# Optimization experiments

Measured on AMD Instinct MI355X. Metric: run time of the kernel, lower is better.

The kernel has to match this reference:

```python
import jax, jax.numpy as jnp
import numpy as np

D, L, C, H, W = 4, 16, 64, 128, 128


def setup_inputs() -> dict:
    key = jax.random.key(0)
    ks = jax.random.split(key, 20)
    rn = lambda k, shape, s=0.02: jax.random.normal(k, shape, dtype=jnp.float32) * s
    return {
        "x": jax.random.normal(ks[0], (L, C, H, W), dtype=jnp.float32),
        "ln1_g": jnp.ones((D, C, H, W), jnp.float32),
        "ln1_b": jnp.zeros((D, C, H, W), jnp.float32),
        "Wq": rn(ks[1], (D, C, C)), "bq": jnp.zeros((D, C), jnp.float32),
        "Wk": rn(ks[2], (D, C, C)), "bk": jnp.zeros((D, C), jnp.float32),
        "Wv": rn(ks[3], (D, C, C)), "bv": jnp.zeros((D, C), jnp.float32),
        "Wa": rn(ks[4], (D, 1, 2 * C, 5, 5)), "ba": jnp.zeros((D, 1), jnp.float32),
        "ln2_g": jnp.ones((D, C, H, W), jnp.float32),
        "ln2_b": jnp.zeros((D, C, H, W), jnp.float32),
        "W1": rn(ks[5], (D, 2 * C, C)), "b1": jnp.zeros((D, 2 * C), jnp.float32),
        "W2": rn(ks[6], (D, C, 2 * C)), "b2": jnp.zeros((D, C), jnp.float32),
    }


def _layernorm(x, g, b):
    # torch nn.LayerNorm([C,H,W]): normalize over last 3 dims per frame, eps=1e-5
    mu = jnp.mean(x, axis=(1, 2, 3), keepdims=True)
    var = jnp.var(x, axis=(1, 2, 3), keepdims=True)
    return (x - mu) * jax.lax.rsqrt(var + 1e-5) * g[None] + b[None]


def _conv5(x, w):
    # x: [L, Cin, H, W], w: [1, Cin, 5, 5] -> [L, 1, H, W], SAME padding (pad=2)
    return jax.lax.conv_general_dilated(
        x, w, window_strides=(1, 1), padding="SAME",
        dimension_numbers=("NCHW", "OIHW", "NCHW"))


def _conv1x1(x, w, b):
    # 1x1 conv == per-pixel linear over channels
    return jnp.einsum("lchw,oc->lohw", x, w) + b[None, :, None, None]


def reference(x, ln1_g, ln1_b, Wq, bq, Wk, bk, Wv, bv, Wa, ba,
              ln2_g, ln2_b, W1, b1, W2, b2):
    depth = ln1_g.shape[0]
    c = Wa.shape[2] // 2
    for d in range(depth):
        # --- pre-norm conv attention (nheads=1) + residual ---
        h = _layernorm(x, ln1_g[d], ln1_b[d])
        Q = _conv1x1(h, Wq[d], bq[d])
        K = _conv1x1(h, Wk[d], bk[d])
        V = _conv1x1(h, Wv[d], bv[d])
        # conv_atten(cat([Q_i, K_j])) is linear in channels: split the 5x5
        # kernel into Q-part and K-part, so H_ij = A_i + B_j + bias.
        A = _conv5(Q, Wa[d, :, :c])[:, 0]   # [L, H, W]
        B = _conv5(K, Wa[d, :, c:])[:, 0]   # [L, H, W]
        S = A[:, None] + B[None, :] + ba[d][0]      # [L, L, H, W]
        P = jax.nn.softmax(S, axis=1)               # softmax over source frames j
        attn = jnp.einsum("ijhw,jchw->ichw", P, V)  # weighted sum of V_j
        x = x + attn
        # --- pre-norm conv FFN + residual ---
        h = _layernorm(x, ln2_g[d], ln2_b[d])
        f = _conv1x1(h, W1[d], b1[d])
        f = jax.nn.leaky_relu(f, 0.01)  # torch LeakyReLU default slope
        f = _conv1x1(f, W2[d], b2[d])
        x = x + f
    return x
```

## Files before the change

### kernel.cpp

```cpp
#include <hip/hip_runtime.h>


#define HW 16384
#define CHW 1048576
#define NB 64

typedef unsigned short u16;
typedef __attribute__((ext_vector_type(8))) short bf16x8;
typedef __attribute__((ext_vector_type(8))) unsigned short u16x8;
typedef __attribute__((ext_vector_type(4))) float f32x4;

static __device__ __forceinline__ u16 f2bf(float f) {
  union { float f; unsigned int u; } v; v.f = f;
  unsigned int r = v.u + 0x7fffu + ((v.u >> 16) & 1u);
  return (u16)(r >> 16);
}
static __device__ __forceinline__ float bf2f(u16 h) {
  union { unsigned int u; float f; } v; v.u = ((unsigned int)h) << 16;
  return v.f;
}
static __device__ __forceinline__ void ln_from_acc_wave(
    const float* acc, int l, int lane, float& mu, float& r) {
  const float invN = 1.f / 1048576.f;
  float2 v = *(const float2*)(acc + lane * 32 + 2 * l);
  float s = v.x, q = v.y;
#pragma unroll
  for (int off = 32; off > 0; off >>= 1) {
    s += __shfl_xor(s, off);
    q += __shfl_xor(q, off);
  }
  mu = s * invN;
  r = rsqrtf(q * invN - mu * mu + 1e-5f);
}

__global__ __launch_bounds__(256) void prep_kernel(
    const float* __restrict__ Wa, const float* __restrict__ Wk,
    const float* __restrict__ Wv, const float* __restrict__ W1,
    const float* __restrict__ W2, u16* __restrict__ w1pk,
    u16* __restrict__ w2pk, u16* __restrict__ wvpk, u16* __restrict__ wepk) {
  int d = blockIdx.x;
  int t = blockIdx.y * 256 + threadIdx.x;
  const int STR = 256 * 16;
  const float* WaK = Wa + ((size_t)d * 128 + 64) * 25;
  const float* Wkd = Wk + d * 4096;
  for (int idx = t; idx < 2048; idx += STR) {
    int frag = idx >> 9, lane = (idx >> 3) & 63, j = idx & 7;
    int mt = frag >> 1, kt = frag & 1;
    int tap = mt * 16 + (lane & 15);
    int ci = kt * 32 + (lane >> 4) * 8 + j;
    float s = 0.f;
    if (tap < 25)
      for (int co = 0; co < 64; ++co)
        s = fmaf(WaK[co * 25 + tap], Wkd[co * 64 + ci], s);
    wepk[d * 2048 + idx] = f2bf(s);
  }
  const float* Wvd = Wv + d * 4096;
  for (int idx = t; idx < 4096; idx += STR) {
    int frag = idx >> 9, lane = (idx >> 3) & 63, j = idx & 7;
    int mt = frag >> 1, kt = frag & 1;
    int co = mt * 16 + (lane & 15);
    int ci = kt * 32 + (lane >> 4) * 8 + j;
    wvpk[d * 4096 + idx] = f2bf(Wvd[co * 64 + ci]);
  }
  const float* W1d = W1 + d * 8192;
  for (int idx = t; idx < 8192; idx += STR) {
    int frag = idx >> 9, lane = (idx >> 3) & 63, j = idx & 7;
    int mt = frag >> 1, kt = frag & 1;
    int o = mt * 16 + (lane & 15);
    int ci = kt * 32 + (lane >> 4) * 8 + j;
    w1pk[d * 8192 + idx] = f2bf(W1d[o * 64 + ci]);
  }
  const float* W2d = W2 + d * 8192;
  for (int idx = t; idx < 8192; idx += STR) {
    int frag = idx >> 9, lane = (idx >> 3) & 63, j = idx & 7;
    int mt2 = frag >> 2, kt2 = frag & 3;
    int c = mt2 * 16 + (lane & 15);
    int o = kt2 * 32 + (lane >> 4) * 8 + j;
    w2pk[d * 8192 + idx] = f2bf(W2d[c * 128 + o]);
  }
}

__global__ __launch_bounds__(256) void stats_kernel(
    const float* __restrict__ xin, float* __restrict__ acc) {
  int tid = threadIdx.x;
  size_t base = (size_t)blockIdx.x * 4096;
  const float4* in4 = (const float4*)(xin + base);
  float s = 0.f, q = 0.f;
#pragma unroll
  for (int k = 0; k < 4; ++k) {
    float4 v = in4[k * 256 + tid];
    s += v.x + v.y + v.z + v.w;
    q = fmaf(v.x, v.x, q); q = fmaf(v.y, v.y, q);
    q = fmaf(v.z, v.z, q); q = fmaf(v.w, v.w, q);
  }
#pragma unroll
  for (int off = 32; off > 0; off >>= 1) {
    s += __shfl_down(s, off); q += __shfl_down(q, off);
  }
  __shared__ float ls[4], lq[4];
  int wave = tid >> 6;
  if ((tid & 63) == 0) { ls[wave] = s; lq[wave] = q; }
  __syncthreads();
  if (tid == 0) {
    int frame = blockIdx.x >> 8;
    int bkt = blockIdx.x & (NB - 1);
    atomicAdd(&acc[bkt * 32 + frame * 2], ls[0] + ls[1] + ls[2] + ls[3]);
    atomicAdd(&acc[bkt * 32 + frame * 2 + 1], lq[0] + lq[1] + lq[2] + lq[3]);
  }
}

__global__ __launch_bounds__(256) void vb_kernel(
    const float* __restrict__ x, const float* __restrict__ g,
    const float* __restrict__ bln, const u16* __restrict__ wvp_g,
    const float* __restrict__ bv, const u16* __restrict__ wep_g,
    const float* __restrict__ accA, float* __restrict__ accBz,
    u16* __restrict__ Vb, u16* __restrict__ T) {
  __shared__ __align__(16) char lds[18432];
  u16* hb = (u16*)lds;
  int tid = threadIdx.x;
  int l = blockIdx.y;
  int p0 = blockIdx.x << 7;
  if (blockIdx.x == 0 && blockIdx.y == 0)
    for (int i = tid; i < NB * 32; i += 256) accBz[i] = 0.f;
  int lane = tid & 63;
  float mu, r;
  ln_from_acc_wave(accA, l, lane, mu, r);

#pragma unroll
  for (int it = 0; it < 2; ++it) {
    int pq = tid & 31, cg = (tid >> 5) + it * 8;
    int px = pq * 4, c0 = cg * 4;
    float vv[4][4];
#pragma unroll
    for (int i = 0; i < 4; ++i) {
      int c = c0 + i;
      size_t gi = (((size_t)l * 64 + c) << 14) + p0 + px;
      int li = (c << 14) + p0 + px;
      float4 xv = *(const float4*)(x + gi);
      float4 gv = *(const float4*)(g + li);
      float4 bb = *(const float4*)(bln + li);
      vv[i][0] = (xv.x - mu) * r * gv.x + bb.x;
      vv[i][1] = (xv.y - mu) * r * gv.y + bb.y;
      vv[i][2] = (xv.z - mu) * r * gv.z + bb.z;
      vv[i][3] = (xv.w - mu) * r * gv.w + bb.w;
    }
#pragma unroll
    for (int k = 0; k < 4; ++k) {
      int row = px + k;
      int col = ((((c0 >> 3) + (row >> 2)) & 7) << 3) | (c0 & 7);
      ushort4 hv;
      hv.x = f2bf(vv[0][k]); hv.y = f2bf(vv[1][k]);
      hv.z = f2bf(vv[2][k]); hv.w = f2bf(vv[3][k]);
      *(ushort4*)(hb + row * 72 + col) = hv;
    }
  }
  __syncthreads();

  int wv = tid >> 6;
  int ln15 = lane & 15, quad = lane >> 4;

  bf16x8 ah[2][2];
#pragma unroll
  for (int mt = 0; mt < 2; ++mt) {
    int px = (wv * 2 + mt) * 16 + ln15;
#pragma unroll
    for (int kt = 0; kt < 2; ++kt) {
      int slot = ((kt * 4 + quad) + (px >> 2)) & 7;
      ah[mt][kt] = *(const bf16x8*)(hb + px * 72 + (slot << 3));
    }
  }
  const bf16x8* wvg = (const bf16x8*)wvp_g;
  const bf16x8* weg = (const bf16x8*)wep_g;

  f32x4 accV[2][4], accT[2][2];
#pragma unroll
  for (int mt = 0; mt < 2; ++mt) {
#pragma unroll
    for (int nt = 0; nt < 4; ++nt) accV[mt][nt] = (f32x4){0.f, 0.f, 0.f, 0.f};
#pragma unroll
    for (int nt = 0; nt < 2; ++nt) accT[mt][nt] = (f32x4){0.f, 0.f, 0.f, 0.f};
  }
#pragma unroll
  for (int nt = 0; nt < 4; ++nt) {
    bf16x8 b0 = wvg[(nt * 2 + 0) * 64 + lane];
    bf16x8 b1w = wvg[(nt * 2 + 1) * 64 + lane];
#pragma unroll
    for (int mt = 0; mt < 2; ++mt) {
      accV[mt][nt] = __builtin_amdgcn_mfma_f32_16x16x32_bf16(
          ah[mt][0], b0, accV[mt][nt], 0, 0, 0);
      accV[mt][nt] = __builtin_amdgcn_mfma_f32_16x16x32_bf16(
          ah[mt][1], b1w, accV[mt][nt], 0, 0, 0);
    }
  }
#pragma unroll
  for (int nt = 0; nt < 2; ++nt) {
    bf16x8 b0 = weg[(nt * 2 + 0) * 64 + lane];
    bf16x8 b1w = weg[(nt * 2 + 1) * 64 + lane];
#pragma unroll
    for (int mt = 0; mt < 2; ++mt) {
      accT[mt][nt] = __builtin_amdgcn_mfma_f32_16x16x32_bf16(
          ah[mt][0], b0, accT[mt][nt], 0, 0, 0);
      accT[mt][nt] = __builtin_amdgcn_mfma_f32_16x16x32_bf16(
          ah[mt][1], b1w, accT[mt][nt], 0, 0, 0);
    }
  }

#pragma unroll
  for (int mt = 0; mt < 2; ++mt) {
    int pxb = p0 + (wv * 2 + mt) * 16 + quad * 4;
#pragma unroll
    for (int nt = 0; nt < 4; ++nt) {
      int c = nt * 16 + ln15;
      float bvc = bv[c];
      ushort4 o;
      o.x = f2bf(accV[mt][nt][0] + bvc);
      o.y = f2bf(accV[mt][nt][1] + bvc);
      o.z = f2bf(accV[mt][nt][2] + bvc);
      o.w = f2bf(accV[mt][nt][3] + bvc);
      *(ushort4*)(Vb + (((size_t)l * 64 + c) << 14) + pxb) = o;
    }
#pragma unroll
    for (int nt = 0; nt < 2; ++nt) {
      int tap = nt * 16 + ln15;
      if (tap < 25) {
        ushort4 o;
        o.x = f2bf(accT[mt][nt][0]); o.y = f2bf(accT[mt][nt][1]);
        o.z = f2bf(accT[mt][nt][2]); o.w = f2bf(accT[mt][nt][3]);
        *(ushort4*)(T + (((size_t)l * 25 + tap) << 14) + pxb) = o;
      }
    }
  }
}

__global__ __launch_bounds__(256) void bconv_kernel(
    const u16* __restrict__ T, float* __restrict__ B) {
  int gid = blockIdx.x * 256 + threadIdx.x;
  int l = gid >> 14, p = gid & 16383;
  int y = p >> 7, xx = p & 127;
  float s = 0.f;
#pragma unroll
  for (int dy = 0; dy < 5; ++dy) {
    int yy = y + dy - 2;
    if (yy < 0 || yy > 127) continue;
#pragma unroll
    for (int dx = 0; dx < 5; ++dx) {
      int xc = xx + dx - 2;
      if (xc < 0 || xc > 127) continue;
      s += bf2f(T[(((size_t)l * 25 + dy * 5 + dx) << 14) + (yy << 7) + xc]);
    }
  }
  B[gid] = s;
}

__global__ __launch_bounds__(256) void attnc_update_kernel(
    const float* __restrict__ x, const u16* __restrict__ Vb,
    const float* __restrict__ B, float* __restrict__ ap,
    float* __restrict__ accB, float* __restrict__ accAz) {
  int tid = threadIdx.x;
  if (blockIdx.x == 0)
    for (int i = tid; i < NB * 32; i += 256) accAz[i] = 0.f;
  int gid = blockIdx.x * 256 + tid;
  int c = gid >> 11;
  int p8 = (gid & 2047) << 3;
  float m[8];
#pragma unroll
  for (int k = 0; k < 8; ++k) m[k] = -1e30f;
#pragma unroll
  for (int j = 0; j < 16; ++j) {
    float4 b0 = *(const float4*)(B + (j << 14) + p8);
    float4 b1 = *(const float4*)(B + (j << 14) + p8 + 4);
    m[0] = fmaxf(m[0], b0.x); m[1] = fmaxf(m[1], b0.y);
    m[2] = fmaxf(m[2], b0.z); m[3] = fmaxf(m[3], b0.w);
    m[4] = fmaxf(m[4], b1.x); m[5] = fmaxf(m[5], b1.y);
    m[6] = fmaxf(m[6], b1.z); m[7] = fmaxf(m[7], b1.w);
  }
  float sum[8], a[8];
#pragma unroll
  for (int k = 0; k < 8; ++k) { sum[k] = 0.f; a[k] = 0.f; }
#pragma unroll
  for (int j = 0; j < 16; ++j) {
    float4 b0 = *(const float4*)(B + (j << 14) + p8);
    float4 b1 = *(const float4*)(B + (j << 14) + p8 + 4);
    float e[8];
    e[0] = __expf(b0.x - m[0]); e[1] = __expf(b0.y - m[1]);
    e[2] = __expf(b0.z - m[2]); e[3] = __expf(b0.w - m[3]);
    e[4] = __expf(b1.x - m[4]); e[5] = __expf(b1.y - m[5]);
    e[6] = __expf(b1.z - m[6]); e[7] = __expf(b1.w - m[7]);
    u16x8 v = *(const u16x8*)(Vb + (((size_t)j * 64 + c) << 14) + p8);
#pragma unroll
    for (int k = 0; k < 8; ++k) {
      sum[k] += e[k];
      a[k] = fmaf(e[k], bf2f(v[k]), a[k]);
    }
  }
#pragma unroll
  for (int k = 0; k < 8; ++k) a[k] /= sum[k];
  float4 a0 = {a[0], a[1], a[2], a[3]};
  float4 a1 = {a[4], a[5], a[6], a[7]};
  *(float4*)(ap + ((size_t)c << 14) + p8) = a0;
  *(float4*)(ap + ((size_t)c << 14) + p8 + 4) = a1;
  float sf[16], qf[16];
#pragma unroll
  for (int f = 0; f < 16; ++f) {
    size_t gi = ((size_t)f << 20) + ((size_t)c << 14) + p8;
    float4 v0 = *(const float4*)(x + gi);
    float4 v1 = *(const float4*)(x + gi + 4);
    v0.x += a0.x; v0.y += a0.y; v0.z += a0.z; v0.w += a0.w;
    v1.x += a1.x; v1.y += a1.y; v1.z += a1.z; v1.w += a1.w;
    sf[f] = v0.x + v0.y + v0.z + v0.w + v1.x + v1.y + v1.z + v1.w;
    float q = 0.f;
    q = fmaf(v0.x, v0.x, q); q = fmaf(v0.y, v0.y, q);
    q = fmaf(v0.z, v0.z, q); q = fmaf(v0.w, v0.w, q);
    q = fmaf(v1.x, v1.x, q); q = fmaf(v1.y, v1.y, q);
    q = fmaf(v1.z, v1.z, q); q = fmaf(v1.w, v1.w, q);
    qf[f] = q;
  }
#pragma unroll
  for (int off = 32; off > 0; off >>= 1) {
#pragma unroll
    for (int f = 0; f < 16; ++f) {
      sf[f] += __shfl_down(sf[f], off);
      qf[f] += __shfl_down(qf[f], off);
    }
  }
  __shared__ float lsq[4][32];
  int wv = tid >> 6;
  if ((tid & 63) == 0) {
#pragma unroll
    for (int f = 0; f < 16; ++f) {
      lsq[wv][2 * f] = sf[f];
      lsq[wv][2 * f + 1] = qf[f];
    }
  }
  __syncthreads();
  if (tid < 32) {
    int bkt = blockIdx.x & (NB - 1);
    atomicAdd(&accB[bkt * 32 + tid],
              lsq[0][tid] + lsq[1][tid] + lsq[2][tid] + lsq[3][tid]);
  }
}

__global__ __launch_bounds__(256) void ffn_kernel(
    const float* __restrict__ xr, float* __restrict__ xw,
    const float* __restrict__ ap, const float* __restrict__ g,
    const float* __restrict__ bln, const u16* __restrict__ w1p_g,
    const float* __restrict__ b1, const u16* __restrict__ w2p_g,
    const float* __restrict__ b2, const float* __restrict__ accB,
    float* __restrict__ accA) {
  __shared__ __align__(16) char lds[66560];
  float* xaf = (float*)lds;
  u16* hb = (u16*)(lds + 33792);
  u16* f1 = (u16*)(lds + 33792);

  int tid = threadIdx.x;
  int P0 = blockIdx.x << 7;
  int l = P0 >> 14;
  int p0 = P0 & 16383;
  int lane = tid & 63;
  float mu, r;
  ln_from_acc_wave(accB, l, lane, mu, r);

#pragma unroll
  for (int it = 0; it < 2; ++it) {
    int pq = tid & 31, cg = (tid >> 5) + it * 8;
    int px = pq * 4, c0 = cg * 4;
    float vv[4][4];
#pragma unroll
    for (int i = 0; i < 4; ++i) {
      int c = c0 + i;
      size_t gi = (((size_t)l * 64 + c) << 14) + p0 + px;
      int li = (c << 14) + p0 + px;
      float4 xv = *(const float4*)(xr + gi);
      float4 av = *(const float4*)(ap + li);
      float4 gv = *(const float4*)(g + li);
      float4 bb = *(const float4*)(bln + li);
      float4 s4;
      s4.x = xv.x + av.x; s4.y = xv.y + av.y;
      s4.z = xv.z + av.z; s4.w = xv.w + av.w;
      *(float4*)(xaf + c * 132 + px) = s4;
      vv[i][0] = (s4.x - mu) * r * gv.x + bb.x;
      vv[i][1] = (s4.y - mu) * r * gv.y + bb.y;
      vv[i][2] = (s4.z - mu) * r * gv.z + bb.z;
      vv[i][3] = (s4.w - mu) * r * gv.w + bb.w;
    }
#pragma unroll
    for (int k = 0; k < 4; ++k) {
      int row = px + k;
      int col = ((((c0 >> 3) + (row >> 2)) & 7) << 3) | (c0 & 7);
      ushort4 hv;
      hv.x = f2bf(vv[0][k]); hv.y = f2bf(vv[1][k]);
      hv.z = f2bf(vv[2][k]); hv.w = f2bf(vv[3][k]);
      *(ushort4*)(hb + row * 72 + col) = hv;
    }
  }
  __syncthreads();

  int wv = tid >> 6;
  int ln15 = lane & 15, quad = lane >> 4;

  bf16x8 bh[2][2];
#pragma unroll
  for (int nt = 0; nt < 2; ++nt) {
    int px = (wv * 2 + nt) * 16 + ln15;
#pragma unroll
    for (int kt = 0; kt < 2; ++kt) {
      int slot = ((kt * 4 + quad) + (px >> 2)) & 7;
      bh[nt][kt] = *(const bf16x8*)(hb + px * 72 + (slot << 3));
    }
  }
  __syncthreads();

  const bf16x8* w1g = (const bf16x8*)w1p_g;
  const bf16x8* w2g = (const bf16x8*)w2p_g;

#pragma unroll
  for (int mt = 0; mt < 8; ++mt) {
    bf16x8 a1a = w1g[(mt * 2 + 0) * 64 + lane];
    bf16x8 a1b = w1g[(mt * 2 + 1) * 64 + lane];
    f32x4 acc[2];
    acc[0] = (f32x4){0.f, 0.f, 0.f, 0.f};
    acc[1] = (f32x4){0.f, 0.f, 0.f, 0.f};
#pragma unroll
    for (int nt = 0; nt < 2; ++nt) {
      acc[nt] = __builtin_amdgcn_mfma_f32_16x16x32_bf16(a1a, bh[nt][0],
                                                        acc[nt], 0, 0, 0);
      acc[nt] = __builtin_amdgcn_mfma_f32_16x16x32_bf16(a1b, bh[nt][1],
                                                        acc[nt], 0, 0, 0);
    }
    int o0 = mt * 16 + quad * 4;
    float4 b1v = *(const float4*)(b1 + o0);
#pragma unroll
    for (int nt = 0; nt < 2; ++nt) {
      int px = (wv * 2 + nt) * 16 + ln15;
      int swz = (px & 7) * 8;
      float fv[4];
#pragma unroll
      for (int rj = 0; rj < 4; ++rj) {
        float f = acc[nt][rj] + ((const float*)&b1v)[rj];
        fv[rj] = fmaxf(f, 0.01f * f);
      }
      int col = ((o0 & ~7) ^ swz) + (o0 & 7);
      ushort4 ov;
      ov.x = f2bf(fv[0]); ov.y = f2bf(fv[1]);
      ov.z = f2bf(fv[2]); ov.w = f2bf(fv[3]);
      *(ushort4*)(f1 + px * 128 + col) = ov;
    }
  }
  __syncthreads();

  bf16x8 a2[2][4];
#pragma unroll
  for (int mt = 0; mt < 2; ++mt) {
    int px = (wv * 2 + mt) * 16 + ln15;
    int swz = (px & 7) * 8;
#pragma unroll
    for (int kt = 0; kt < 4; ++kt)
      a2[mt][kt] =
          *(const bf16x8*)(f1 + px * 128 + ((kt * 32 + quad * 8) ^ swz));
  }
  f32x4 acc2[2][4];
#pragma unroll
  for (int mt = 0; mt < 2; ++mt)
#pragma unroll
    for (int nt = 0; nt < 4; ++nt) acc2[mt][nt] = (f32x4){0.f, 0.f, 0.f, 0.f};
#pragma unroll
  for (int nt = 0; nt < 4; ++nt) {
    bf16x8 bw[4];
#pragma unroll
    for (int kt = 0; kt < 4; ++kt) bw[kt] = w2g[(nt * 4 + kt) * 64 + lane];
#pragma unroll
    for (int mt = 0; mt < 2; ++mt)
#pragma unroll
      for (int kt = 0; kt < 4; ++kt)
        acc2[mt][nt] = __builtin_amdgcn_mfma_f32_16x16x32_bf16(
            a2[mt][kt], bw[kt], acc2[mt][nt], 0, 0, 0);
  }

  float s = 0.f, q = 0.f;
#pragma unroll
  for (int mt = 0; mt < 2; ++mt) {
    int pxl = (wv * 2 + mt) * 16 + quad * 4;
#pragma unroll
    for (int nt = 0; nt < 4; ++nt) {
      int c = nt * 16 + ln15;
      float b2c = b2[c];
      const float* xac = xaf + c * 132 + pxl;
      float4 v;
      v.x = xac[0] + acc2[mt][nt][0] + b2c;
      v.y = xac[1] + acc2[mt][nt][1] + b2c;
      v.z = xac[2] + acc2[mt][nt][2] + b2c;
      v.w = xac[3] + acc2[mt][nt][3] + b2c;
      *(float4*)(xw + (((size_t)l * 64 + c) << 14) + p0 + pxl) = v;
      s += v.x + v.y + v.z + v.w;
      q = fmaf(v.x, v.x, q); q = fmaf(v.y, v.y, q);
      q = fmaf(v.z, v.z, q); q = fmaf(v.w, v.w, q);
    }
  }
#pragma unroll
  for (int off = 32; off > 0; off >>= 1) {
    s += __shfl_down(s, off); q += __shfl_down(q, off);
  }
  if (lane == 0) {
    int bkt = blockIdx.x & (NB - 1);
    atomicAdd(&accA[bkt * 32 + l * 2], s);
    atomicAdd(&accA[bkt * 32 + l * 2 + 1], q);
  }
}

extern "C" void kernel_launch(void* const* d_in, const int* in_sizes, int n_in,
                              void* d_out, int out_size, void* d_ws,
                              size_t ws_size, hipStream_t stream) {
  const float* x_in = (const float*)d_in[0];
  const float* ln1_g = (const float*)d_in[1];
  const float* ln1_b = (const float*)d_in[2];
  const float* Wk = (const float*)d_in[5];
  const float* Wv = (const float*)d_in[7];
  const float* bv = (const float*)d_in[8];
  const float* Wa = (const float*)d_in[9];
  const float* ln2_g = (const float*)d_in[11];
  const float* ln2_b = (const float*)d_in[12];
  const float* W1 = (const float*)d_in[13];
  const float* b1 = (const float*)d_in[14];
  const float* W2 = (const float*)d_in[15];
  const float* b2 = (const float*)d_in[16];

  float* xbuf = (float*)d_out;
  char* wsb = (char*)d_ws;
  u16* Vb = (u16*)wsb;
  u16* T = (u16*)(wsb + 33554432);
  float* aplane = (float*)(wsb + 46661632);
  float* Bbuf = (float*)(wsb + 50855936);
  u16* w1pk = (u16*)(wsb + 51904512);
  u16* w2pk = (u16*)(wsb + 51970048);
  u16* wvpk = (u16*)(wsb + 52035584);
  u16* wepk = (u16*)(wsb + 52068352);
  float* accA = (float*)(wsb + 52084736);
  float* accB = (float*)(wsb + 52092928);

  hipMemsetAsync(accA, 0, 16384, stream);
  prep_kernel<<<dim3(4, 16), 256, 0, stream>>>(Wa, Wk, Wv, W1, W2, w1pk, w2pk,
                                               wvpk, wepk);
  stats_kernel<<<4096, 256, 0, stream>>>(x_in, accA);

  const float* xr = x_in;
  for (int d = 0; d < 4; ++d) {
    vb_kernel<<<dim3(128, 16), 256, 0, stream>>>(
        xr, ln1_g + (size_t)d * CHW, ln1_b + (size_t)d * CHW, wvpk + d * 4096,
        bv + d * 64, wepk + d * 2048, accA, accB, Vb, T);
    bconv_kernel<<<1024, 256, 0, stream>>>(T, Bbuf);
    attnc_update_kernel<<<512, 256, 0, stream>>>(xr, Vb, Bbuf, aplane, accB,
                                                 accA);
    ffn_kernel<<<2048, 256, 0, stream>>>(
        xr, xbuf, aplane, ln2_g + (size_t)d * CHW, ln2_b + (size_t)d * CHW,
        w1pk + d * 8192, b1 + d * 128, w2pk + d * 8192, b2 + d * 64, accB,
        accA);
    xr = xbuf;
  }
}
```

Measured before the change: 598.8 us.

## Apply softmax weights before V projection and store LN params in bf16

```diff
diff --git a/kernel.cpp b/kernel.cpp
--- a/kernel.cpp
+++ b/kernel.cpp
@@ -80,6 +80,26 @@
   }
 }
 
+__global__ __launch_bounds__(256) void lngb_kernel(
+    const float* __restrict__ g1, const float* __restrict__ b1,
+    const float* __restrict__ g2, const float* __restrict__ b2,
+    u16* __restrict__ o1, u16* __restrict__ o2, u16* __restrict__ o3,
+    u16* __restrict__ o4) {
+  int idx = blockIdx.x * 256 + threadIdx.x;
+  const float* src;
+  u16* dst;
+  switch (blockIdx.y) {
+    case 0: src = g1; dst = o1; break;
+    case 1: src = b1; dst = o2; break;
+    case 2: src = g2; dst = o3; break;
+    default: src = b2; dst = o4; break;
+  }
+  float4 v = *(const float4*)(src + (size_t)idx * 4);
+  ushort4 o;
+  o.x = f2bf(v.x); o.y = f2bf(v.y); o.z = f2bf(v.z); o.w = f2bf(v.w);
+  *(ushort4*)(dst + (size_t)idx * 4) = o;
+}
+
 __global__ __launch_bounds__(256) void stats_kernel(
     const float* __restrict__ xin, float* __restrict__ acc) {
   int tid = threadIdx.x;
@@ -109,12 +129,11 @@
   }
 }
 
-__global__ __launch_bounds__(256) void vb_kernel(
-    const float* __restrict__ x, const float* __restrict__ g,
-    const float* __restrict__ bln, const u16* __restrict__ wvp_g,
-    const float* __restrict__ bv, const u16* __restrict__ wep_g,
+__global__ __launch_bounds__(256) void tb_kernel(
+    const float* __restrict__ x, const u16* __restrict__ g,
+    const u16* __restrict__ bln, const u16* __restrict__ wep_g,
     const float* __restrict__ accA, float* __restrict__ accBz,
-    u16* __restrict__ Vb, u16* __restrict__ T) {
+    float* __restrict__ mulr, u16* __restrict__ T) {
   __shared__ __align__(16) char lds[18432];
   u16* hb = (u16*)lds;
   int tid = threadIdx.x;
@@ -125,6 +144,10 @@
   int lane = tid & 63;
   float mu, r;
   ln_from_acc_wave(accA, l, lane, mu, r);
+  if (blockIdx.x == 0 && tid == 0) {
+    mulr[2 * l] = mu;
+    mulr[2 * l + 1] = r;
+  }
 
 #pragma unroll
   for (int it = 0; it < 2; ++it) {
@@ -137,12 +160,12 @@
       size_t gi = (((size_t)l * 64 + c) << 14) + p0 + px;
       int li = (c << 14) + p0 + px;
       float4 xv = *(const float4*)(x + gi);
-      float4 gv = *(const float4*)(g + li);
-      float4 bb = *(const float4*)(bln + li);
-      vv[i][0] = (xv.x - mu) * r * gv.x + bb.x;
-      vv[i][1] = (xv.y - mu) * r * gv.y + bb.y;
-      vv[i][2] = (xv.z - mu) * r * gv.z + bb.z;
-      vv[i][3] = (xv.w - mu) * r * gv.w + bb.w;
+      ushort4 gv = *(const ushort4*)(g + li);
+      ushort4 bb = *(const ushort4*)(bln + li);
+      vv[i][0] = (xv.x - mu) * r * bf2f(gv.x) + bf2f(bb.x);
+      vv[i][1] = (xv.y - mu) * r * bf2f(gv.y) + bf2f(bb.y);
+      vv[i][2] = (xv.z - mu) * r * bf2f(gv.z) + bf2f(bb.z);
+      vv[i][3] = (xv.w - mu) * r * bf2f(gv.w) + bf2f(bb.w);
     }
 #pragma unroll
     for (int k = 0; k < 4; ++k) {
@@ -169,29 +192,13 @@
       ah[mt][kt] = *(const bf16x8*)(hb + px * 72 + (slot << 3));
     }
   }
-  const bf16x8* wvg = (const bf16x8*)wvp_g;
   const bf16x8* weg = (const bf16x8*)wep_g;
 
-  f32x4 accV[2][4], accT[2][2];
-#pragma unroll
-  for (int mt = 0; mt < 2; ++mt) {
-#pragma unroll
-    for (int nt = 0; nt < 4; ++nt) accV[mt][nt] = (f32x4){0.f, 0.f, 0.f, 0.f};
+  f32x4 accT[2][2];
+#pragma unroll
+  for (int mt = 0; mt < 2; ++mt)
 #pragma unroll
     for (int nt = 0; nt < 2; ++nt) accT[mt][nt] = (f32x4){0.f, 0.f, 0.f, 0.f};
-  }
-#pragma unroll
-  for (int nt = 0; nt < 4; ++nt) {
-    bf16x8 b0 = wvg[(nt * 2 + 0) * 64 + lane];
-    bf16x8 b1w = wvg[(nt * 2 + 1) * 64 + lane];
-#pragma unroll
-    for (int mt = 0; mt < 2; ++mt) {
-      accV[mt][nt] = __builtin_amdgcn_mfma_f32_16x16x32_bf16(
-          ah[mt][0], b0, accV[mt][nt], 0, 0, 0);
-      accV[mt][nt] = __builtin_amdgcn_mfma_f32_16x16x32_bf16(
-          ah[mt][1], b1w, accV[mt][nt], 0, 0, 0);
-    }
-  }
 #pragma unroll
   for (int nt = 0; nt < 2; ++nt) {
     bf16x8 b0 = weg[(nt * 2 + 0) * 64 + lane];
@@ -208,17 +215,6 @@
 #pragma unroll
   for (int mt = 0; mt < 2; ++mt) {
     int pxb = p0 + (wv * 2 + mt) * 16 + quad * 4;
-#pragma unroll
-    for (int nt = 0; nt < 4; ++nt) {
-      int c = nt * 16 + ln15;
-      float bvc = bv[c];
-      ushort4 o;
-      o.x = f2bf(accV[mt][nt][0] + bvc);
-      o.y = f2bf(accV[mt][nt][1] + bvc);
-      o.z = f2bf(accV[mt][nt][2] + bvc);
-      o.w = f2bf(accV[mt][nt][3] + bvc);
-      *(ushort4*)(Vb + (((size_t)l * 64 + c) << 14) + pxb) = o;
-    }
 #pragma unroll
     for (int nt = 0; nt < 2; ++nt) {
       int tap = nt * 16 + ln15;
@@ -252,68 +248,139 @@
   B[gid] = s;
 }
 
-__global__ __launch_bounds__(256) void attnc_update_kernel(
-    const float* __restrict__ x, const u16* __restrict__ Vb,
-    const float* __restrict__ B, float* __restrict__ ap,
+__global__ __launch_bounds__(256) void attnc_kernel(
+    const float* __restrict__ x, const float* __restrict__ B,
+    const u16* __restrict__ g1, const u16* __restrict__ b1g,
+    const u16* __restrict__ wvp_g, const float* __restrict__ bv,
+    const float* __restrict__ mulr, u16* __restrict__ abf,
     float* __restrict__ accB, float* __restrict__ accAz) {
+  __shared__ float Prl[16][64];
+  __shared__ float scal[64];
+  __shared__ __align__(16) u16 hb[64 * 72];
+  __shared__ float lsq[4][32];
   int tid = threadIdx.x;
+  int p0 = blockIdx.x << 6;
   if (blockIdx.x == 0)
     for (int i = tid; i < NB * 32; i += 256) accAz[i] = 0.f;
-  int gid = blockIdx.x * 256 + tid;
-  int c = gid >> 11;
-  int p8 = (gid & 2047) << 3;
-  float m[8];
-#pragma unroll
-  for (int k = 0; k < 8; ++k) m[k] = -1e30f;
+
+  if (tid < 64) {
+    float bj[16], m = -1e30f;
+#pragma unroll
+    for (int j = 0; j < 16; ++j) {
+      bj[j] = B[(j << 14) + p0 + tid];
+      m = fmaxf(m, bj[j]);
+    }
+    float sum = 0.f;
+#pragma unroll
+    for (int j = 0; j < 16; ++j) {
+      bj[j] = __expf(bj[j] - m);
+      sum += bj[j];
+    }
+    float inv = 1.f / sum;
+    float sc = 0.f;
+#pragma unroll
+    for (int j = 0; j < 16; ++j) {
+      float mu_j = mulr[2 * j], r_j = mulr[2 * j + 1];
+      float prl = bj[j] * inv * r_j;
+      Prl[j][tid] = prl;
+      sc = fmaf(prl, mu_j, sc);
+    }
+    scal[tid] = sc;
+  }
+  __syncthreads();
+
+  int csub = tid >> 4, pxq = tid & 15;
+  f32x4 xbar[4];
+#pragma unroll
+  for (int cc = 0; cc < 4; ++cc) xbar[cc] = (f32x4){0.f, 0.f, 0.f, 0.f};
 #pragma unroll
   for (int j = 0; j < 16; ++j) {
-    float4 b0 = *(const float4*)(B + (j << 14) + p8);
-    float4 b1 = *(const float4*)(B + (j << 14) + p8 + 4);
-    m[0] = fmaxf(m[0], b0.x); m[1] = fmaxf(m[1], b0.y);
-    m[2] = fmaxf(m[2], b0.z); m[3] = fmaxf(m[3], b0.w);
-    m[4] = fmaxf(m[4], b1.x); m[5] = fmaxf(m[5], b1.y);
-    m[6] = fmaxf(m[6], b1.z); m[7] = fmaxf(m[7], b1.w);
-  }
-  float sum[8], a[8];
-#pragma unroll
-  for (int k = 0; k < 8; ++k) { sum[k] = 0.f; a[k] = 0.f; }
-#pragma unroll
-  for (int j = 0; j < 16; ++j) {
-    float4 b0 = *(const float4*)(B + (j << 14) + p8);
-    float4 b1 = *(const float4*)(B + (j << 14) + p8 + 4);
-    float e[8];
-    e[0] = __expf(b0.x - m[0]); e[1] = __expf(b0.y - m[1]);
-    e[2] = __expf(b0.z - m[2]); e[3] = __expf(b0.w - m[3]);
-    e[4] = __expf(b1.x - m[4]); e[5] = __expf(b1.y - m[5]);
-    e[6] = __expf(b1.z - m[6]); e[7] = __expf(b1.w - m[7]);
-    u16x8 v = *(const u16x8*)(Vb + (((size_t)j * 64 + c) << 14) + p8);
-#pragma unroll
-    for (int k = 0; k < 8; ++k) {
-      sum[k] += e[k];
-      a[k] = fmaf(e[k], bf2f(v[k]), a[k]);
-    }
-  }
-#pragma unroll
-  for (int k = 0; k < 8; ++k) a[k] /= sum[k];
-  float4 a0 = {a[0], a[1], a[2], a[3]};
-  float4 a1 = {a[4], a[5], a[6], a[7]};
-  *(float4*)(ap + ((size_t)c << 14) + p8) = a0;
-  *(float4*)(ap + ((size_t)c << 14) + p8 + 4) = a1;
+    f32x4 P4 = *(const f32x4*)&Prl[j][pxq * 4];
+#pragma unroll
+    for (int cc = 0; cc < 4; ++cc) {
+      int c = cc * 16 + csub;
+      float4 xv =
+          *(const float4*)(x + (((size_t)j * 64 + c) << 14) + p0 + pxq * 4);
+      xbar[cc][0] = fmaf(P4[0], xv.x, xbar[cc][0]);
+      xbar[cc][1] = fmaf(P4[1], xv.y, xbar[cc][1]);
+      xbar[cc][2] = fmaf(P4[2], xv.z, xbar[cc][2]);
+      xbar[cc][3] = fmaf(P4[3], xv.w, xbar[cc][3]);
+    }
+  }
+  {
+    f32x4 sc4 = *(const f32x4*)&scal[pxq * 4];
+#pragma unroll
+    for (int cc = 0; cc < 4; ++cc) {
+      int c = cc * 16 + csub;
+      ushort4 g4 = *(const ushort4*)(g1 + ((size_t)c << 14) + p0 + pxq * 4);
+      ushort4 b4 = *(const ushort4*)(b1g + ((size_t)c << 14) + p0 + pxq * 4);
+      float hv[4];
+      hv[0] = bf2f(g4.x) * (xbar[cc][0] - sc4[0]) + bf2f(b4.x);
+      hv[1] = bf2f(g4.y) * (xbar[cc][1] - sc4[1]) + bf2f(b4.y);
+      hv[2] = bf2f(g4.z) * (xbar[cc][2] - sc4[2]) + bf2f(b4.z);
+      hv[3] = bf2f(g4.w) * (xbar[cc][3] - sc4[3]) + bf2f(b4.w);
+#pragma unroll
+      for (int k = 0; k < 4; ++k) {
+        int row = pxq * 4 + k;
+        int col = ((((c >> 3) + (row >> 2)) & 7) << 3) | (c & 7);
+        hb[row * 72 + col] = f2bf(hv[k]);
+      }
+    }
+  }
+  __syncthreads();
+
+  int wv = tid >> 6, lane = tid & 63;
+  int ln15 = lane & 15, quad = lane >> 4;
+  int px = wv * 16 + ln15;
+  bf16x8 ah[2];
+#pragma unroll
+  for (int kt = 0; kt < 2; ++kt) {
+    int slot = ((kt * 4 + quad) + (px >> 2)) & 7;
+    ah[kt] = *(const bf16x8*)(hb + px * 72 + (slot << 3));
+  }
+  const bf16x8* wvg = (const bf16x8*)wvp_g;
+  f32x4 accV[4];
+#pragma unroll
+  for (int nt = 0; nt < 4; ++nt) accV[nt] = (f32x4){0.f, 0.f, 0.f, 0.f};
+#pragma unroll
+  for (int nt = 0; nt < 4; ++nt) {
+    bf16x8 b0 = wvg[(nt * 2 + 0) * 64 + lane];
+    bf16x8 b1w = wvg[(nt * 2 + 1) * 64 + lane];
+    accV[nt] = __builtin_amdgcn_mfma_f32_16x16x32_bf16(ah[0], b0, accV[nt],
+                                                       0, 0, 0);
+    accV[nt] = __builtin_amdgcn_mfma_f32_16x16x32_bf16(ah[1], b1w, accV[nt],
+                                                       0, 0, 0);
+  }
+  int pxb = p0 + wv * 16 + quad * 4;
+  float av[4][4];
+#pragma unroll
+  for (int nt = 0; nt < 4; ++nt) {
+    int c = nt * 16 + ln15;
+    float bvc = bv[c];
+    ushort4 o;
+    av[nt][0] = accV[nt][0] + bvc; o.x = f2bf(av[nt][0]);
+    av[nt][1] = accV[nt][1] + bvc; o.y = f2bf(av[nt][1]);
+    av[nt][2] = accV[nt][2] + bvc; o.z = f2bf(av[nt][2]);
+    av[nt][3] = accV[nt][3] + bvc; o.w = f2bf(av[nt][3]);
+    *(ushort4*)(abf + ((size_t)c << 14) + pxb) = o;
+  }
+
   float sf[16], qf[16];
 #pragma unroll
   for (int f = 0; f < 16; ++f) {
-    size_t gi = ((size_t)f << 20) + ((size_t)c << 14) + p8;
-    float4 v0 = *(const float4*)(x + gi);
-    float4 v1 = *(const float4*)(x + gi + 4);
-    v0.x += a0.x; v0.y += a0.y; v0.z += a0.z; v0.w += a0.w;
-    v1.x += a1.x; v1.y += a1.y; v1.z += a1.z; v1.w += a1.w;
-    sf[f] = v0.x + v0.y + v0.z + v0.w + v1.x + v1.y + v1.z + v1.w;
-    float q = 0.f;
-    q = fmaf(v0.x, v0.x, q); q = fmaf(v0.y, v0.y, q);
-    q = fmaf(v0.z, v0.z, q); q = fmaf(v0.w, v0.w, q);
-    q = fmaf(v1.x, v1.x, q); q = fmaf(v1.y, v1.y, q);
-    q = fmaf(v1.z, v1.z, q); q = fmaf(v1.w, v1.w, q);
-    qf[f] = q;
+    float s = 0.f, q = 0.f;
+#pragma unroll
+    for (int nt = 0; nt < 4; ++nt) {
+      int c = nt * 16 + ln15;
+      float4 xv =
+          *(const float4*)(x + ((size_t)f << 20) + ((size_t)c << 14) + pxb);
+      float v0 = xv.x + av[nt][0], v1 = xv.y + av[nt][1];
+      float v2 = xv.z + av[nt][2], v3 = xv.w + av[nt][3];
+      s += v0 + v1 + v2 + v3;
+      q = fmaf(v0, v0, q); q = fmaf(v1, v1, q);
+      q = fmaf(v2, v2, q); q = fmaf(v3, v3, q);
+    }
+    sf[f] = s; qf[f] = q;
   }
 #pragma unroll
   for (int off = 32; off > 0; off >>= 1) {
@@ -323,9 +390,7 @@
       qf[f] += __shfl_down(qf[f], off);
     }
   }
-  __shared__ float lsq[4][32];
-  int wv = tid >> 6;
-  if ((tid & 63) == 0) {
+  if (lane == 0) {
 #pragma unroll
     for (int f = 0; f < 16; ++f) {
       lsq[wv][2 * f] = sf[f];
@@ -342,8 +407,8 @@
 
 __global__ __launch_bounds__(256) void ffn_kernel(
     const float* __restrict__ xr, float* __restrict__ xw,
-    const float* __restrict__ ap, const float* __restrict__ g,
-    const float* __restrict__ bln, const u16* __restrict__ w1p_g,
+    const u16* __restrict__ ap, const u16* __restrict__ g,
+    const u16* __restrict__ bln, const u16* __restrict__ w1p_g,
     const float* __restrict__ b1, const u16* __restrict__ w2p_g,
     const float* __restrict__ b2, const float* __restrict__ accB,
     float* __restrict__ accA) {
@@ -371,17 +436,17 @@
       size_t gi = (((size_t)l * 64 + c) << 14) + p0 + px;
       int li = (c << 14) + p0 + px;
       float4 xv = *(const float4*)(xr + gi);
-      float4 av = *(const float4*)(ap + li);
-      float4 gv = *(const float4*)(g + li);
-      float4 bb = *(const float4*)(bln + li);
+      ushort4 av4 = *(const ushort4*)(ap + li);
+      ushort4 gv = *(const ushort4*)(g + li);
+      ushort4 bb = *(const ushort4*)(bln + li);
       float4 s4;
-      s4.x = xv.x + av.x; s4.y = xv.y + av.y;
-      s4.z = xv.z + av.z; s4.w = xv.w + av.w;
+      s4.x = xv.x + bf2f(av4.x); s4.y = xv.y + bf2f(av4.y);
+      s4.z = xv.z + bf2f(av4.z); s4.w = xv.w + bf2f(av4.w);
       *(float4*)(xaf + c * 132 + px) = s4;
-      vv[i][0] = (s4.x - mu) * r * gv.x + bb.x;
-      vv[i][1] = (s4.y - mu) * r * gv.y + bb.y;
-      vv[i][2] = (s4.z - mu) * r * gv.z + bb.z;
-      vv[i][3] = (s4.w - mu) * r * gv.w + bb.w;
+      vv[i][0] = (s4.x - mu) * r * bf2f(gv.x) + bf2f(bb.x);
+      vv[i][1] = (s4.y - mu) * r * bf2f(gv.y) + bf2f(bb.y);
+      vv[i][2] = (s4.z - mu) * r * bf2f(gv.z) + bf2f(bb.z);
+      vv[i][3] = (s4.w - mu) * r * bf2f(gv.w) + bf2f(bb.w);
     }
 #pragma unroll
     for (int k = 0; k < 4; ++k) {
@@ -526,32 +591,39 @@
 
   float* xbuf = (float*)d_out;
   char* wsb = (char*)d_ws;
-  u16* Vb = (u16*)wsb;
-  u16* T = (u16*)(wsb + 33554432);
-  float* aplane = (float*)(wsb + 46661632);
-  float* Bbuf = (float*)(wsb + 50855936);
-  u16* w1pk = (u16*)(wsb + 51904512);
-  u16* w2pk = (u16*)(wsb + 51970048);
-  u16* wvpk = (u16*)(wsb + 52035584);
-  u16* wepk = (u16*)(wsb + 52068352);
-  float* accA = (float*)(wsb + 52084736);
-  float* accB = (float*)(wsb + 52092928);
+  u16* T = (u16*)wsb;
+  u16* abf = (u16*)(wsb + 13107200);
+  float* Bbuf = (float*)(wsb + 15204352);
+  u16* g1b = (u16*)(wsb + 16252928);
+  u16* b1bb = (u16*)(wsb + 24641536);
+  u16* g2b = (u16*)(wsb + 33030144);
+  u16* b2bb = (u16*)(wsb + 41418752);
+  u16* w1pk = (u16*)(wsb + 49807360);
+  u16* w2pk = (u16*)(wsb + 49872896);
+  u16* wvpk = (u16*)(wsb + 49938432);
+  u16* wepk = (u16*)(wsb + 49971200);
+  float* mulr = (float*)(wsb + 49987584);
+  float* accA = (float*)(wsb + 49987712);
+  float* accB = (float*)(wsb + 49995904);
 
   hipMemsetAsync(accA, 0, 16384, stream);
   prep_kernel<<<dim3(4, 16), 256, 0, stream>>>(Wa, Wk, Wv, W1, W2, w1pk, w2pk,
                                                wvpk, wepk);
+  lngb_kernel<<<dim3(4096, 4), 256, 0, stream>>>(ln1_g, ln1_b, ln2_g, ln2_b,
+                                                 g1b, b1bb, g2b, b2bb);
   stats_kernel<<<4096, 256, 0, stream>>>(x_in, accA);
 
   const float* xr = x_in;
   for (int d = 0; d < 4; ++d) {
-    vb_kernel<<<dim3(128, 16), 256, 0, stream>>>(
-        xr, ln1_g + (size_t)d * CHW, ln1_b + (size_t)d * CHW, wvpk + d * 4096,
-        bv + d * 64, wepk + d * 2048, accA, accB, Vb, T);
+    tb_kernel<<<dim3(128, 16), 256, 0, stream>>>(
+        xr, g1b + (size_t)d * CHW, b1bb + (size_t)d * CHW, wepk + d * 2048,
+        accA, accB, mulr, T);
     bconv_kernel<<<1024, 256, 0, stream>>>(T, Bbuf);
-    attnc_update_kernel<<<512, 256, 0, stream>>>(xr, Vb, Bbuf, aplane, accB,
-                                                 accA);
+    attnc_kernel<<<256, 256, 0, stream>>>(
+        xr, Bbuf, g1b + (size_t)d * CHW, b1bb + (size_t)d * CHW,
+        wvpk + d * 4096, bv + d * 64, mulr, abf, accB, accA);
     ffn_kernel<<<2048, 256, 0, stream>>>(
-        xr, xbuf, aplane, ln2_g + (size_t)d * CHW, ln2_b + (size_t)d * CHW,
+        xr, xbuf, abf, g2b + (size_t)d * CHW, b2bb + (size_t)d * CHW,
         w1pk + d * 8192, b1 + d * 128, w2pk + d * 8192, b2 + d * 64, accB,
         accA);
     xr = xbuf;
```

Result: faster. 565.2 us (-5.6%).
